# Kernel tuning notes

Measured on AMD Instinct MI355X. Metric: run time of the kernel, lower is better.

Reference implementation:

```python
import jax, jax.numpy as jnp
import numpy as np

NUM_HEADS = 8
SCALE = 25.0
SIM_THRESH = 0.75


def setup_inputs() -> dict:
    key = jax.random.key(0)
    ks = jax.random.split(key, 6)
    B, N, C = 1, 2048, 1024
    x_cls = jax.random.normal(ks[0], (B, N, C), jnp.float32)
    x_reg = jax.random.normal(ks[1], (B, N, C), jnp.float32)
    cls_score = jax.random.uniform(ks[2], (N,), jnp.float32)
    fg_score = jax.random.uniform(ks[3], (N,), jnp.float32)
    W_qkv_cls = jax.random.normal(ks[4], (3 * C, C), jnp.float32) * 0.02
    W_qkv_reg = jax.random.normal(ks[5], (3 * C, C), jnp.float32) * 0.02
    return {"x_cls": x_cls, "x_reg": x_reg, "cls_score": cls_score,
            "fg_score": fg_score, "W_qkv_cls": W_qkv_cls, "W_qkv_reg": W_qkv_reg}


def _l2norm(t):
    return t / jnp.linalg.norm(t, axis=-1, keepdims=True)


def reference(x_cls, x_reg, cls_score, fg_score, W_qkv_cls, W_qkv_reg):
    B, N, C = x_cls.shape
    H = NUM_HEADS
    d = C // H

    def qkv(x, W):
        # (B,N,3C) -> (3,B,H,N,d)
        t = (x @ W.T).reshape(B, N, 3, H, d).transpose(2, 0, 3, 1, 4)
        return t[0], t[1], t[2]

    q_cls, k_cls, v_cls = qkv(x_cls, W_qkv_cls)
    q_reg, k_reg, _ = qkv(x_reg, W_qkv_reg)

    q_cls, k_cls = _l2norm(q_cls), _l2norm(k_cls)
    q_reg, k_reg = _l2norm(q_reg), _l2norm(k_reg)
    v_cls_normed = _l2norm(v_cls)

    # scores broadcast: s[..., i, j] = score[j]; transpose -> score[i]
    s_cls = cls_score.reshape(1, 1, 1, N)
    s_fg = fg_score.reshape(1, 1, 1, N)
    # use_mask=True branch
    m_cls = (s_cls > jnp.swapaxes(s_cls, -2, -1) - 0.1).astype(x_cls.dtype)
    m_fg = (s_fg > jnp.swapaxes(s_fg, -2, -1) - 0.1).astype(x_cls.dtype)

    attn_cls_raw = jnp.einsum('bhid,bhjd->bhij', v_cls_normed, v_cls_normed)

    attn_cls = jax.nn.softmax(
        jnp.einsum('bhid,bhjd->bhij', q_cls, k_cls) * SCALE * s_cls * m_cls, axis=-1)
    attn_reg = jax.nn.softmax(
        jnp.einsum('bhid,bhjd->bhij', q_reg, k_reg) * SCALE * s_fg * m_fg, axis=-1)
    attn = (attn_reg + attn_cls) * 0.5

    x = jnp.einsum('bhij,bhjd->bhid', attn, v_cls).transpose(0, 2, 1, 3).reshape(B, N, C)
    x_ori = v_cls.transpose(0, 2, 1, 3).reshape(B, N, C)
    x_out = jnp.concatenate([x, x_ori], axis=-1)  # (B, N, 2C)

    # ave=True branch (batch 0, head-mean)
    raw = attn_cls_raw.sum(axis=1)[0] / H  # (N, N)
    sim_mask = (raw > SIM_THRESH).astype(x_cls.dtype)
    sim_attn = attn.sum(axis=1)[0] / H
    sim_round2 = jax.nn.softmax(sim_attn, axis=-1)
    sim_round2 = sim_mask * sim_round2
    sim_round2 = sim_round2 / jnp.sum(sim_round2, axis=-1, keepdims=True)
    return x_out, sim_round2
```

## Files before the change

kernel.cpp:

```cpp
#include <hip/hip_runtime.h>


#define NTOK 2048
#define CDIM 1024

typedef __attribute__((ext_vector_type(8))) short bf16x8;
typedef __attribute__((ext_vector_type(4))) short s16x4;
typedef __attribute__((ext_vector_type(2))) short s16x2;
typedef __attribute__((ext_vector_type(4))) float f32x4;

#define MFMA16(a,b,c) __builtin_amdgcn_mfma_f32_16x16x32_bf16((a),(b),(c),0,0,0)

__device__ __forceinline__ short f2bf(float x){
  unsigned u = __float_as_uint(x);
  u += 0x7FFFu + ((u >> 16) & 1u);
  return (short)(u >> 16);
}

__device__ __forceinline__ float bf2f(short s){
  return __uint_as_float(((unsigned)(unsigned short)s) << 16);
}

__device__ __forceinline__ int cvtpk(float lo, float hi){
  int r;
  asm("v_cvt_pk_bf16_f32 %0, %1, %2" : "=v"(r) : "v"(lo), "v"(hi));
  return r;
}

__device__ __forceinline__ void atomAddF(float* p, float v){
  unsafeAtomicAdd(p, v);
}

__device__ __forceinline__ void gld16(const short* g, short* l){
  __builtin_amdgcn_global_load_lds(
      (const __attribute__((address_space(1))) unsigned int*)g,
      (__attribute__((address_space(3))) unsigned int*)l, 16, 0, 0);
}

__global__ __launch_bounds__(256,8) void k_cvt(
    const float* __restrict__ xc, const float* __restrict__ xr,
    const float* __restrict__ Wc, const float* __restrict__ Wr,
    short* __restrict__ xbc, short* __restrict__ xbr,
    short* __restrict__ wbc, short* __restrict__ wbr)
{
  int idx = blockIdx.x*256 + threadIdx.x;
  const float* src; short* dst; int off;
  if      (idx <  262144){ src = xc; dst = xbc; off = idx; }
  else if (idx <  524288){ src = xr; dst = xbr; off = idx - 262144; }
  else if (idx <  917504){ src = Wc; dst = wbc; off = idx - 524288; }
  else                   { src = Wr; dst = wbr; off = idx - 917504; }
  float4 a = *(const float4*)(src + (size_t)off*8);
  float4 b = *(const float4*)(src + (size_t)off*8 + 4);
  bf16x8 o = { f2bf(a.x), f2bf(a.y), f2bf(a.z), f2bf(a.w),
               f2bf(b.x), f2bf(b.y), f2bf(b.z), f2bf(b.w) };
  *(bf16x8*)(dst + (size_t)off*8) = o;
}

__global__ __launch_bounds__(256,3) void k_qkv(
    const short* __restrict__ xbc, const short* __restrict__ xbr,
    const short* __restrict__ wbc, const short* __restrict__ wbr,
    short* __restrict__ qc, short* __restrict__ kc,
    short* __restrict__ qr, short* __restrict__ kr,
    short* __restrict__ vn, short* __restrict__ vb,
    float* __restrict__ out)
{
  const int tid = threadIdx.x;
  const int l   = tid & 63;
  const int w   = tid >> 6;
  const int fr  = l & 15;
  const int g   = l >> 4;
  const int fk8 = g * 8;

  const int L     = blockIdx.x;
  const int xcd   = L & 7;
  const int slot  = L >> 3;
  const int panel = xcd*5 + (slot >> 4);
  const int mb    = slot & 15;
  const int m0    = mb * 128;
  const int o0    = panel * 128;

  const short* Xb; const short* Wb; int wrow;
  if (o0 < 3072){ Xb = xbc; Wb = wbc; wrow = o0; }
  else          { Xb = xbr; Wb = wbr; wrow = o0 - 3072; }

  __shared__ __align__(16) short Ab[2][8][64][8];
  __shared__ __align__(16) short Bb[2][8][64][8];
  __shared__ float nbuf[128][2];

  const int wr = w >> 1;
  const int wc = w & 1;

#define QSTAGE(DB, KN) do {                                                  \
    _Pragma("unroll")                                                        \
    for (int it=0; it<2; ++it){                                              \
      int f = it*4 + w;                                                      \
      gld16(Xb + (size_t)(m0  + f*16 + fr)*CDIM + (KN) + fk8,                \
            &Ab[DB][f][0][0]);                                               \
      gld16(Wb + (size_t)(wrow + f*16 + fr)*CDIM + (KN) + fk8,               \
            &Bb[DB][f][0][0]);                                               \
    }                                                                        \
  } while(0)

  f32x4 acc[4][4] = {};

  QSTAGE(0, 0);
  __syncthreads();

  for (int kt = 0; kt < 32; ++kt){
    const int db = kt & 1;
    if (kt < 31){ if (db) QSTAGE(0, (kt+1)*32); else QSTAGE(1, (kt+1)*32); }
    bf16x8 af[4], bfr[4];
    #pragma unroll
    for (int ai=0;ai<4;ai++) af[ai]  = *(const bf16x8*)&Ab[db][wr*4+ai][l][0];
    #pragma unroll
    for (int bj=0;bj<4;bj++) bfr[bj] = *(const bf16x8*)&Bb[db][wc*4+bj][l][0];
    #pragma unroll
    for (int ai=0;ai<4;ai++)
      #pragma unroll
      for (int bj=0;bj<4;bj++)
        acc[ai][bj] = MFMA16(af[ai], bfr[bj], acc[ai][bj]);
    __syncthreads();
  }
#undef QSTAGE

  const int chunk = o0 >> 10;
  const int hh    = (o0 >> 7) & 7;

  float rn[4][4];
  #pragma unroll
  for (int ai=0;ai<4;ai++)
    #pragma unroll
    for (int r=0;r<4;r++){
      float ss = 0.f;
      #pragma unroll
      for (int bj=0;bj<4;bj++) ss += acc[ai][bj][r]*acc[ai][bj][r];
      ss += __shfl_xor(ss, 1); ss += __shfl_xor(ss, 2);
      ss += __shfl_xor(ss, 4); ss += __shfl_xor(ss, 8);
      if (fr == 0) nbuf[wr*64 + ai*16 + g*4 + r][wc] = ss;
      rn[ai][r] = ss;
    }
  __syncthreads();
  #pragma unroll
  for (int ai=0;ai<4;ai++)
    #pragma unroll
    for (int r=0;r<4;r++){
      int row = wr*64 + ai*16 + g*4 + r;
      rn[ai][r] = rsqrtf(nbuf[row][0] + nbuf[row][1]);
    }

  #pragma unroll
  for (int ai=0;ai<4;ai++)
    #pragma unroll
    for (int r=0;r<4;r++){
      int n   = m0 + wr*64 + ai*16 + g*4 + r;
      size_t base = ((size_t)hh*NTOK + n)*128;
      #pragma unroll
      for (int bj=0;bj<4;bj++){
        int col = wc*64 + bj*16 + fr;
        float val = acc[ai][bj][r];
        short nv  = f2bf(val * rn[ai][r]);
        switch(chunk){
          case 0: qc[base+col] = nv; break;
          case 1: kc[base+col] = nv; break;
          case 3: qr[base+col] = nv; break;
          case 4: kr[base+col] = nv; break;
          default:
            vn[base+col] = nv;
            vb[base+col] = f2bf(val);
            out[(size_t)n*2048 + 1024 + hh*128 + col] = val;
            break;
        }
      }
    }
}

__global__ __launch_bounds__(256,4) void k_vT(
    const short* __restrict__ vb, short* __restrict__ vT)
{
  int b = blockIdx.x;
  int h  = b >> 6;
  int nt = (b >> 1) & 31;
  int dt = b & 1;
  __shared__ short t[64][72];
  int tid = threadIdx.x;
  int r  = tid >> 2;
  int c0 = (tid & 3) << 4;
  #pragma unroll
  for (int u=0;u<2;u++){
    bf16x8 val = *(const bf16x8*)&vb[((size_t)h*NTOK + nt*64 + r)*128 + dt*64 + c0 + u*8];
    #pragma unroll
    for (int e=0;e<8;e++) t[r][c0+u*8+e] = val[e];
  }
  __syncthreads();
  #pragma unroll
  for (int u=0;u<2;u++){
    bf16x8 o;
    #pragma unroll
    for (int e=0;e<8;e++) o[e] = t[c0+u*8+e][r];
    *(bf16x8*)&vT[((size_t)h*128 + dt*64 + r)*NTOK + nt*64 + c0 + u*8] = o;
  }
}

#define JLEN 1024

__global__ __launch_bounds__(256,2) void k_attn(
    const short* __restrict__ qc, const short* __restrict__ kc,
    const short* __restrict__ qr, const short* __restrict__ kr,
    const short* __restrict__ vT,
    const float* __restrict__ csc, const float* __restrict__ fsc,
    float* __restrict__ s_cls, float* __restrict__ s_reg,
    short* __restrict__ Up)
{
  const int tid = threadIdx.x;
  const int l   = tid & 63;
  const int w   = tid >> 6;
  const int L    = blockIdx.x;
  const int xcd  = L & 7;
  const int slot = L >> 3;
  const int hs   = ((slot >> 5) << 3) | xcd;
  const int h    = hs >> 1;
  const int s    = hs & 1;
  const int rem  = slot & 31;
  const int js   = rem >> 4;
  const int ib   = rem & 15;

  const int iw  = ib * 128 + w * 32;
  const int fr  = l & 15;
  const int g   = l >> 4;
  const int fk8 = g * 8;
  const size_t hN = (size_t)h * NTOK;
  const size_t hD = (size_t)h * 128;

  const short* Qp = s ? qr : qc;
  const short* Kp = s ? kr : kc;
  const float* sc = s ? fsc : csc;
  float* ssum     = s ? s_reg : s_cls;
  short* Ub       = Up + (size_t)(js*2 + s) * 2097152;

  __shared__ __align__(16) short Kbuf[2][4][4][64][8];
  __shared__ __align__(16) short Vbuf[2][8][2][64][8];

  const int t8 = w * 8;

#define STAGE(DB, JN) do {                                                   \
    _Pragma("unroll")                                                        \
    for (int q8=0; q8<8; ++q8){                                              \
      int t = t8 + q8;                                                       \
      if (t < 16){                                                           \
        int jf = t >> 2, kk = t & 3;                                         \
        gld16(Kp + (hN + (JN) + jf*16 + fr)*128 + kk*32 + fk8,               \
              &Kbuf[DB][jf][kk][0][0]);                                      \
      } else {                                                               \
        int u = t - 16, df = u >> 1, ks = u & 1;                             \
        gld16(vT + (hD + df*16 + fr)*2048 + (JN) + ks*32 + fk8,              \
              &Vbuf[DB][df][ks][0][0]);                                      \
      }                                                                      \
    }                                                                        \
  } while(0)

  bf16x8 bq[2][4];
  #pragma unroll
  for (int i2=0;i2<2;i2++)
    #pragma unroll
    for (int kk=0;kk<4;kk++)
      bq[i2][kk] = *(const bf16x8*)&Qp[(hN + iw + i2*16 + fr)*128 + kk*32 + fk8];

  float sci[2];
  sci[0] = sc[iw + fr] - 0.1f;
  sci[1] = sc[iw + 16 + fr] - 0.1f;

  f32x4 U[2][8] = {};
  float p[2] = {0.f, 0.f};

  const int srcA = ((((g<<1)    & 3) << 4) + fr) << 2;
  const int srcB = ((((g<<1 | 1)& 3) << 4) + fr) << 2;
  const bool ghi = g >= 2;
  const int jbase = js * JLEN;

  STAGE(0, jbase);
  __syncthreads();

  for (int jt = 0; jt < 16; ++jt){
    const int db = jt & 1;
    const int j0 = jbase + jt*64;
    if (jt < 15){ if (db) STAGE(0, j0 + 64); else STAGE(1, j0 + 64); }
    #pragma unroll
    for (int ks=0; ks<2; ++ks){
      int cpk[2][2][2];
      #pragma unroll
      for (int t=0; t<2; ++t){
        const int jf = ks*2 + t;
        f32x4 S0 = {}; f32x4 S1 = {};
        __builtin_amdgcn_s_setprio(1);
        #pragma unroll
        for (int kk=0; kk<4; ++kk){
          bf16x8 kb = *(const bf16x8*)&Kbuf[db][jf][kk][l][0];
          S0 = MFMA16(kb, bq[0][kk], S0);
          S1 = MFMA16(kb, bq[1][kk], S1);
        }
        __builtin_amdgcn_s_setprio(0);
        float4 sjv = *(const float4*)&sc[j0 + jf*16 + 4*g];
        float e0[4], e1[4];
        #pragma unroll
        for (int r=0;r<4;r++){
          float sj = (&sjv.x)[r];
          float sj25 = 25.0f * sj;
          e0[r] = (sj > sci[0]) ? __expf(S0[r]*sj25) : 1.0f;
          e1[r] = (sj > sci[1]) ? __expf(S1[r]*sj25) : 1.0f;
          p[0] += e0[r]; p[1] += e1[r];
        }
        cpk[0][t][0] = cvtpk(e0[0], e0[1]);
        cpk[0][t][1] = cvtpk(e0[2], e0[3]);
        cpk[1][t][0] = cvtpk(e1[0], e1[1]);
        cpk[1][t][1] = cvtpk(e1[2], e1[3]);
      }
      bf16x8 ea[2];
      #pragma unroll
      for (int i2=0;i2<2;i2++){
        int a0 = __builtin_amdgcn_ds_bpermute(srcA, cpk[i2][0][0]);
        int a1 = __builtin_amdgcn_ds_bpermute(srcA, cpk[i2][0][1]);
        int a2 = __builtin_amdgcn_ds_bpermute(srcA, cpk[i2][1][0]);
        int a3 = __builtin_amdgcn_ds_bpermute(srcA, cpk[i2][1][1]);
        int b0 = __builtin_amdgcn_ds_bpermute(srcB, cpk[i2][0][0]);
        int b1 = __builtin_amdgcn_ds_bpermute(srcB, cpk[i2][0][1]);
        int b2 = __builtin_amdgcn_ds_bpermute(srcB, cpk[i2][1][0]);
        int b3 = __builtin_amdgcn_ds_bpermute(srcB, cpk[i2][1][1]);
        int wd[4];
        wd[0] = ghi ? a2 : a0;  wd[1] = ghi ? a3 : a1;
        wd[2] = ghi ? b2 : b0;  wd[3] = ghi ? b3 : b1;
        ea[i2] = *(bf16x8*)wd;
      }
      __builtin_amdgcn_s_setprio(1);
      #pragma unroll
      for (int df=0; df<8; ++df){
        bf16x8 bv = *(const bf16x8*)&Vbuf[db][df][ks][l][0];
        U[0][df] = MFMA16(ea[0], bv, U[0][df]);
        U[1][df] = MFMA16(ea[1], bv, U[1][df]);
      }
      __builtin_amdgcn_s_setprio(0);
    }
    __syncthreads();
  }
#undef STAGE

  #pragma unroll
  for (int i2=0;i2<2;i2++){
    p[i2] += __shfl_xor(p[i2], 16);
    p[i2] += __shfl_xor(p[i2], 32);
  }
  if (l < 16){
    atomAddF(&ssum[hN + iw + l],      p[0]);
    atomAddF(&ssum[hN + iw + 16 + l], p[1]);
  }
  #pragma unroll
  for (int i2=0;i2<2;i2++)
    #pragma unroll
    for (int df=0;df<8;df++)
      #pragma unroll
      for (int r=0;r<4;r++)
        Ub[(hN + iw + i2*16 + g*4 + r)*128 + df*16 + fr] = f2bf(U[i2][df][r]);
}

__global__ __launch_bounds__(256,8) void k_attn_fin(
    const short* __restrict__ Up,
    const float* __restrict__ s_cls, const float* __restrict__ s_reg,
    float* __restrict__ out)
{
  int task = blockIdx.x*4 + (threadIdx.x>>6);
  int lane = threadIdx.x & 63;
  int h = task >> 11;
  int row = task & 2047;
  size_t b = (size_t)task*128 + lane*2;
  float cx=0.f, cy=0.f, rx=0.f, ry=0.f;
  #pragma unroll
  for (int js=0; js<2; ++js){
    s16x2 c = *(const s16x2*)(Up + (size_t)(js*2+0)*2097152 + b);
    s16x2 r = *(const s16x2*)(Up + (size_t)(js*2+1)*2097152 + b);
    cx += bf2f(c[0]); cy += bf2f(c[1]);
    rx += bf2f(r[0]); ry += bf2f(r[1]);
  }
  float isc = 0.5f/s_cls[task];
  float isr = 0.5f/s_reg[task];
  float2 o = { cx*isc + rx*isr, cy*isc + ry*isr };
  *(float2*)&out[(size_t)row*2048 + h*128 + lane*2] = o;
}

__global__ __launch_bounds__(256,2) void k_sim(
    const short* __restrict__ qc, const short* __restrict__ kc,
    const short* __restrict__ qr, const short* __restrict__ kr,
    const float* __restrict__ csc, const float* __restrict__ fsc,
    const float* __restrict__ s_cls, const float* __restrict__ s_reg,
    float* __restrict__ out)
{
  const int tid  = threadIdx.x;
  const int lane = tid & 63;
  const int w    = tid >> 6;
  const int i0w  = blockIdx.x * 128 + w * 32;
  const int j0   = blockIdx.y * 64;
  const int fr   = lane & 15;
  const int fk   = (lane >> 4) * 8;

  __shared__ __align__(16) short Bsh[2][16][64][8];

  float sjc[4], sjf[4];
  #pragma unroll
  for (int js=0;js<4;js++){ sjc[js]=csc[j0+js*16+fr]; sjf[js]=fsc[j0+js*16+fr]; }
  int rowb[2]; float sci[2][4], sfi[2][4];
  #pragma unroll
  for (int ri=0;ri<2;ri++){
    rowb[ri] = i0w + ri*16 + ((lane>>4)<<2);
    #pragma unroll
    for (int r=0;r<4;r++){ sci[ri][r]=csc[rowb[ri]+r]; sfi[ri][r]=fsc[rowb[ri]+r]; }
  }

  f32x4 sim[2][4] = {};

  for (int h=0; h<8; ++h){
    const size_t hb = (size_t)h * NTOK;
    bf16x8 aq[2][4], ar[2][4];
    #pragma unroll
    for (int ri=0;ri<2;ri++)
      #pragma unroll
      for (int kk=0;kk<4;kk++){
        aq[ri][kk] = *(const bf16x8*)&qc[(hb + i0w + ri*16 + fr)*128 + kk*32 + fk];
        ar[ri][kk] = *(const bf16x8*)&qr[(hb + i0w + ri*16 + fr)*128 + kk*32 + fk];
      }
    float iscl[2][4], isrl[2][4];
    #pragma unroll
    for (int ri=0;ri<2;ri++)
      #pragma unroll
      for (int r=0;r<4;r++){
        iscl[ri][r] = 1.0f/s_cls[hb + rowb[ri] + r];
        isrl[ri][r] = 1.0f/s_reg[hb + rowb[ri] + r];
      }
    __syncthreads();
    #pragma unroll
    for (int it=0; it<8; ++it){
      int slot = it*256 + tid;
      int str  = slot >> 10;
      int frag = (slot >> 6) & 15;
      int l    = slot & 63;
      int r    = (frag >> 2)*16 + (l & 15);
      int c    = (frag & 3)*32 + (l >> 4)*8;
      const short* gp = (str ? kr : kc) + (hb + j0 + r)*128 + c;
      *(bf16x8*)&Bsh[str][frag][l][0] = *(const bf16x8*)gp;
    }
    __syncthreads();
    #pragma unroll
    for (int js=0; js<4; ++js){
      bf16x8 bc[4], br[4];
      #pragma unroll
      for (int kk=0;kk<4;kk++){
        bc[kk] = *(const bf16x8*)&Bsh[0][js*4+kk][lane][0];
        br[kk] = *(const bf16x8*)&Bsh[1][js*4+kk][lane][0];
      }
      #pragma unroll
      for (int ri=0;ri<2;ri++){
        f32x4 Sc = {}; f32x4 Sr = {};
        #pragma unroll
        for (int kk=0;kk<4;kk++){
          Sc = MFMA16(aq[ri][kk], bc[kk], Sc);
          Sr = MFMA16(ar[ri][kk], br[kk], Sr);
        }
        #pragma unroll
        for (int r=0;r<4;r++){
          float ec = (sjc[js] > sci[ri][r]-0.1f) ? __expf(Sc[r]*(25.0f*sjc[js])) : 1.0f;
          float er = (sjf[js] > sfi[ri][r]-0.1f) ? __expf(Sr[r]*(25.0f*sjf[js])) : 1.0f;
          sim[ri][js][r] += ec*iscl[ri][r] + er*isrl[ri][r];
        }
      }
    }
  }
  #pragma unroll
  for (int ri=0;ri<2;ri++)
    #pragma unroll
    for (int js=0;js<4;js++)
      #pragma unroll
      for (int r=0;r<4;r++)
        out[4194304ull + (size_t)(rowb[ri]+r)*2048 + j0 + js*16 + fr]
            = sim[ri][js][r] * 0.0625f;
}

__global__ __launch_bounds__(256,4) void k_raw(
    const short* __restrict__ vn, unsigned char* __restrict__ mask)
{
  const int tid  = threadIdx.x;
  const int lane = tid & 63;
  const int w    = tid >> 6;
  const int i0w  = blockIdx.x * 128 + w * 32;
  const int j0   = blockIdx.y * 64;
  const int fr   = lane & 15;
  const int fk   = (lane >> 4) * 8;

  __shared__ __align__(16) short Bsh[16][64][8];

  f32x4 raw[2][4] = {};

  for (int cc=0; cc<8; ++cc){
    const size_t hb = (size_t)cc * NTOK;
    bf16x8 av[2][4];
    #pragma unroll
    for (int ri=0;ri<2;ri++)
      #pragma unroll
      for (int kk=0;kk<4;kk++)
        av[ri][kk] = *(const bf16x8*)&vn[(hb + i0w + ri*16 + fr)*128 + kk*32 + fk];
    __syncthreads();
    #pragma unroll
    for (int it=0; it<4; ++it){
      int slot = it*256 + tid;
      int frag = (slot >> 6) & 15;
      int l    = slot & 63;
      int r    = (frag >> 2)*16 + (l & 15);
      int c    = (frag & 3)*32 + (l >> 4)*8;
      *(bf16x8*)&Bsh[frag][l][0] = *(const bf16x8*)&vn[(hb + j0 + r)*128 + c];
    }
    __syncthreads();
    #pragma unroll
    for (int js=0; js<4; ++js){
      bf16x8 bv[4];
      #pragma unroll
      for (int kk=0;kk<4;kk++) bv[kk] = *(const bf16x8*)&Bsh[js*4+kk][lane][0];
      #pragma unroll
      for (int ri=0;ri<2;ri++)
        #pragma unroll
        for (int kk=0;kk<4;kk++)
          raw[ri][js] = MFMA16(av[ri][kk], bv[kk], raw[ri][js]);
    }
  }
  const int rb0 = i0w + ((lane>>4)<<2);
  #pragma unroll
  for (int ri=0;ri<2;ri++)
    #pragma unroll
    for (int js=0;js<4;js++)
      #pragma unroll
      for (int r=0;r<4;r++)
        mask[(size_t)(rb0 + ri*16 + r)*2048 + j0 + js*16 + fr]
            = raw[ri][js][r] > 6.0f ? 1 : 0;
}

__global__ __launch_bounds__(256,4) void k_final(
    float* __restrict__ out, const unsigned char* __restrict__ mask)
{
  int row  = blockIdx.x*4 + (threadIdx.x>>6);
  int lane = threadIdx.x & 63;
  float* sr = out + 4194304ull + (size_t)row*2048;
  const unsigned char* mr = mask + (size_t)row*2048;
  float v[32];
  float sum2 = 0.0f;
  #pragma unroll
  for (int c=0;c<32;c++){
    float e = __expf(sr[c*64 + lane]);
    v[c] = (mr[c*64 + lane] != 0) ? e : 0.0f;
    sum2 += v[c];
  }
  #pragma unroll
  for (int m=1;m<64;m<<=1) sum2 += __shfl_xor(sum2, m);
  float inv = 1.0f / sum2;
  #pragma unroll
  for (int c=0;c<32;c++) sr[c*64 + lane] = v[c]*inv;
}

extern "C" void kernel_launch(void* const* d_in, const int* in_sizes, int n_in,
                              void* d_out, int out_size, void* d_ws, size_t ws_size,
                              hipStream_t stream)
{
  const float* xcls = (const float*)d_in[0];
  const float* xreg = (const float*)d_in[1];
  const float* csc  = (const float*)d_in[2];
  const float* fsc  = (const float*)d_in[3];
  const float* Wc   = (const float*)d_in[4];
  const float* Wr   = (const float*)d_in[5];
  float* out = (float*)d_out;

  char* ws = (char*)d_ws;
  short* xbc = (short*)ws;
  short* xbr = xbc + 2097152;
  short* wbc = xbr + 2097152;
  short* wbr = wbc + 3145728;
  unsigned char* mask = (unsigned char*)ws;
  char* accbase       = ws + 4u*1024*1024;
  float* s_cls        = (float*)(accbase);
  float* s_reg        = (float*)(accbase + 65536);
  short* Up           = (short*)(accbase + 131072);
  short* qc = (short*)(ws + 41943040ull);
  short* kc = qc + 2097152;
  short* qr = kc + 2097152;
  short* kr = qr + 2097152;
  short* vn = kr + 2097152;
  short* vb = vn + 2097152;
  short* vT = vb + 2097152;

  k_cvt  <<<4608,        256, 0, stream>>>(xcls, xreg, Wc, Wr, xbc, xbr, wbc, wbr);
  k_qkv  <<<640,         256, 0, stream>>>(xbc, xbr, wbc, wbr,
                                           qc, kc, qr, kr, vn, vb, out);
  k_vT   <<<512,         256, 0, stream>>>(vb, vT);
  hipMemsetAsync(accbase, 0, 131072, stream);
  k_attn <<<512,         256, 0, stream>>>(qc, kc, qr, kr, vT, csc, fsc,
                                           s_cls, s_reg, Up);
  k_attn_fin <<<4096,    256, 0, stream>>>(Up, s_cls, s_reg, out);
  k_raw  <<<dim3(16,32), 256, 0, stream>>>(vn, mask);
  k_sim  <<<dim3(16,32), 256, 0, stream>>>(qc, kc, qr, kr, csc, fsc, s_cls, s_reg, out);
  k_final<<<512,         256, 0, stream>>>(out, mask);
}
```

Measured before the change: 250.0 us.

## Fuse raw similarity mask into k_sim and widen k_attn to 8 waves

Removes the separate k_raw kernel by computing the V·V raw-similarity MFMAs inside k_sim, which now stages a third B tile (vn) in shared memory and writes the mask alongside the sim output. This drops a launch and reuses the existing tile loop and A-fragment loads. k_attn goes from 256 to 512 threads, each wave now owning 16 query rows instead of 32, with staging split over 8 waves. That should raise occupancy, but each K/V tile now feeds only one MFMA row block per load, and k_sim uses more registers and shared memory.

```diff
diff --git a/kernel.cpp b/kernel.cpp
--- a/kernel.cpp
+++ b/kernel.cpp
@@ -203,7 +203,7 @@
 
 #define JLEN 1024
 
-__global__ __launch_bounds__(256,2) void k_attn(
+__global__ __launch_bounds__(512,4) void k_attn(
     const short* __restrict__ qc, const short* __restrict__ kc,
     const short* __restrict__ qr, const short* __restrict__ kr,
     const short* __restrict__ vT,
@@ -224,7 +224,7 @@
   const int js   = rem >> 4;
   const int ib   = rem & 15;
 
-  const int iw  = ib * 128 + w * 32;
+  const int iw  = ib * 128 + w * 16;
   const int fr  = l & 15;
   const int g   = l >> 4;
   const int fk8 = g * 8;
@@ -240,12 +240,12 @@
   __shared__ __align__(16) short Kbuf[2][4][4][64][8];
   __shared__ __align__(16) short Vbuf[2][8][2][64][8];
 
-  const int t8 = w * 8;
+  const int t4 = w * 4;
 
 #define STAGE(DB, JN) do {                                                   \
     _Pragma("unroll")                                                        \
-    for (int q8=0; q8<8; ++q8){                                              \
-      int t = t8 + q8;                                                       \
+    for (int q4=0; q4<4; ++q4){                                              \
+      int t = t4 + q4;                                                       \
       if (t < 16){                                                           \
         int jf = t >> 2, kk = t & 3;                                         \
         gld16(Kp + (hN + (JN) + jf*16 + fr)*128 + kk*32 + fk8,               \
@@ -258,19 +258,15 @@
     }                                                                        \
   } while(0)
 
-  bf16x8 bq[2][4];
-  #pragma unroll
-  for (int i2=0;i2<2;i2++)
-    #pragma unroll
-    for (int kk=0;kk<4;kk++)
-      bq[i2][kk] = *(const bf16x8*)&Qp[(hN + iw + i2*16 + fr)*128 + kk*32 + fk8];
-
-  float sci[2];
-  sci[0] = sc[iw + fr] - 0.1f;
-  sci[1] = sc[iw + 16 + fr] - 0.1f;
-
-  f32x4 U[2][8] = {};
-  float p[2] = {0.f, 0.f};
+  bf16x8 bq[4];
+  #pragma unroll
+  for (int kk=0;kk<4;kk++)
+    bq[kk] = *(const bf16x8*)&Qp[(hN + iw + fr)*128 + kk*32 + fk8];
+
+  const float sci = sc[iw + fr] - 0.1f;
+
+  f32x4 U[8] = {};
+  float p = 0.f;
 
   const int srcA = ((((g<<1)    & 3) << 4) + fr) << 2;
   const int srcB = ((((g<<1 | 1)& 3) << 4) + fr) << 2;
@@ -286,56 +282,47 @@
     if (jt < 15){ if (db) STAGE(0, j0 + 64); else STAGE(1, j0 + 64); }
     #pragma unroll
     for (int ks=0; ks<2; ++ks){
-      int cpk[2][2][2];
+      int cpk[2][2];
       #pragma unroll
       for (int t=0; t<2; ++t){
         const int jf = ks*2 + t;
-        f32x4 S0 = {}; f32x4 S1 = {};
+        f32x4 S0 = {};
         __builtin_amdgcn_s_setprio(1);
         #pragma unroll
         for (int kk=0; kk<4; ++kk){
           bf16x8 kb = *(const bf16x8*)&Kbuf[db][jf][kk][l][0];
-          S0 = MFMA16(kb, bq[0][kk], S0);
-          S1 = MFMA16(kb, bq[1][kk], S1);
+          S0 = MFMA16(kb, bq[kk], S0);
         }
         __builtin_amdgcn_s_setprio(0);
         float4 sjv = *(const float4*)&sc[j0 + jf*16 + 4*g];
-        float e0[4], e1[4];
+        float e0[4];
         #pragma unroll
         for (int r=0;r<4;r++){
           float sj = (&sjv.x)[r];
           float sj25 = 25.0f * sj;
-          e0[r] = (sj > sci[0]) ? __expf(S0[r]*sj25) : 1.0f;
-          e1[r] = (sj > sci[1]) ? __expf(S1[r]*sj25) : 1.0f;
-          p[0] += e0[r]; p[1] += e1[r];
+          e0[r] = (sj > sci) ? __expf(S0[r]*sj25) : 1.0f;
+          p += e0[r];
         }
-        cpk[0][t][0] = cvtpk(e0[0], e0[1]);
-        cpk[0][t][1] = cvtpk(e0[2], e0[3]);
-        cpk[1][t][0] = cvtpk(e1[0], e1[1]);
-        cpk[1][t][1] = cvtpk(e1[2], e1[3]);
-      }
-      bf16x8 ea[2];
-      #pragma unroll
-      for (int i2=0;i2<2;i2++){
-        int a0 = __builtin_amdgcn_ds_bpermute(srcA, cpk[i2][0][0]);
-        int a1 = __builtin_amdgcn_ds_bpermute(srcA, cpk[i2][0][1]);
-        int a2 = __builtin_amdgcn_ds_bpermute(srcA, cpk[i2][1][0]);
-        int a3 = __builtin_amdgcn_ds_bpermute(srcA, cpk[i2][1][1]);
-        int b0 = __builtin_amdgcn_ds_bpermute(srcB, cpk[i2][0][0]);
-        int b1 = __builtin_amdgcn_ds_bpermute(srcB, cpk[i2][0][1]);
-        int b2 = __builtin_amdgcn_ds_bpermute(srcB, cpk[i2][1][0]);
-        int b3 = __builtin_amdgcn_ds_bpermute(srcB, cpk[i2][1][1]);
-        int wd[4];
-        wd[0] = ghi ? a2 : a0;  wd[1] = ghi ? a3 : a1;
-        wd[2] = ghi ? b2 : b0;  wd[3] = ghi ? b3 : b1;
-        ea[i2] = *(bf16x8*)wd;
-      }
+        cpk[t][0] = cvtpk(e0[0], e0[1]);
+        cpk[t][1] = cvtpk(e0[2], e0[3]);
+      }
+      int a0 = __builtin_amdgcn_ds_bpermute(srcA, cpk[0][0]);
+      int a1 = __builtin_amdgcn_ds_bpermute(srcA, cpk[0][1]);
+      int a2 = __builtin_amdgcn_ds_bpermute(srcA, cpk[1][0]);
+      int a3 = __builtin_amdgcn_ds_bpermute(srcA, cpk[1][1]);
+      int b0 = __builtin_amdgcn_ds_bpermute(srcB, cpk[0][0]);
+      int b1 = __builtin_amdgcn_ds_bpermute(srcB, cpk[0][1]);
+      int b2 = __builtin_amdgcn_ds_bpermute(srcB, cpk[1][0]);
+      int b3 = __builtin_amdgcn_ds_bpermute(srcB, cpk[1][1]);
+      int wd[4];
+      wd[0] = ghi ? a2 : a0;  wd[1] = ghi ? a3 : a1;
+      wd[2] = ghi ? b2 : b0;  wd[3] = ghi ? b3 : b1;
+      bf16x8 ea = *(bf16x8*)wd;
       __builtin_amdgcn_s_setprio(1);
       #pragma unroll
       for (int df=0; df<8; ++df){
         bf16x8 bv = *(const bf16x8*)&Vbuf[db][df][ks][l][0];
-        U[0][df] = MFMA16(ea[0], bv, U[0][df]);
-        U[1][df] = MFMA16(ea[1], bv, U[1][df]);
+        U[df] = MFMA16(ea, bv, U[df]);
       }
       __builtin_amdgcn_s_setprio(0);
     }
@@ -343,22 +330,15 @@
   }
 #undef STAGE
 
-  #pragma unroll
-  for (int i2=0;i2<2;i2++){
-    p[i2] += __shfl_xor(p[i2], 16);
-    p[i2] += __shfl_xor(p[i2], 32);
-  }
-  if (l < 16){
-    atomAddF(&ssum[hN + iw + l],      p[0]);
-    atomAddF(&ssum[hN + iw + 16 + l], p[1]);
-  }
-  #pragma unroll
-  for (int i2=0;i2<2;i2++)
-    #pragma unroll
-    for (int df=0;df<8;df++)
-      #pragma unroll
-      for (int r=0;r<4;r++)
-        Ub[(hN + iw + i2*16 + g*4 + r)*128 + df*16 + fr] = f2bf(U[i2][df][r]);
+  p += __shfl_xor(p, 16);
+  p += __shfl_xor(p, 32);
+  if (l < 16)
+    atomAddF(&ssum[hN + iw + l], p);
+  #pragma unroll
+  for (int df=0;df<8;df++)
+    #pragma unroll
+    for (int r=0;r<4;r++)
+      Ub[(hN + iw + g*4 + r)*128 + df*16 + fr] = f2bf(U[df][r]);
 }
 
 __global__ __launch_bounds__(256,8) void k_attn_fin(
@@ -388,9 +368,10 @@
 __global__ __launch_bounds__(256,2) void k_sim(
     const short* __restrict__ qc, const short* __restrict__ kc,
     const short* __restrict__ qr, const short* __restrict__ kr,
+    const short* __restrict__ vn,
     const float* __restrict__ csc, const float* __restrict__ fsc,
     const float* __restrict__ s_cls, const float* __restrict__ s_reg,
-    float* __restrict__ out)
+    unsigned char* __restrict__ mask, float* __restrict__ out)
 {
   const int tid  = threadIdx.x;
   const int lane = tid & 63;
@@ -400,7 +381,7 @@
   const int fr   = lane & 15;
   const int fk   = (lane >> 4) * 8;
 
-  __shared__ __align__(16) short Bsh[2][16][64][8];
+  __shared__ __align__(16) short Bsh[3][16][64][8];
 
   float sjc[4], sjf[4];
   #pragma unroll
@@ -414,16 +395,18 @@
   }
 
   f32x4 sim[2][4] = {};
+  f32x4 raw[2][4] = {};
 
   for (int h=0; h<8; ++h){
     const size_t hb = (size_t)h * NTOK;
-    bf16x8 aq[2][4], ar[2][4];
+    bf16x8 aq[2][4], ar[2][4], av[2][4];
     #pragma unroll
     for (int ri=0;ri<2;ri++)
       #pragma unroll
       for (int kk=0;kk<4;kk++){
         aq[ri][kk] = *(const bf16x8*)&qc[(hb + i0w + ri*16 + fr)*128 + kk*32 + fk];
         ar[ri][kk] = *(const bf16x8*)&qr[(hb + i0w + ri*16 + fr)*128 + kk*32 + fk];
+        av[ri][kk] = *(const bf16x8*)&vn[(hb + i0w + ri*16 + fr)*128 + kk*32 + fk];
       }
     float iscl[2][4], isrl[2][4];
     #pragma unroll
@@ -435,24 +418,25 @@
       }
     __syncthreads();
     #pragma unroll
-    for (int it=0; it<8; ++it){
+    for (int it=0; it<12; ++it){
       int slot = it*256 + tid;
       int str  = slot >> 10;
       int frag = (slot >> 6) & 15;
       int l    = slot & 63;
       int r    = (frag >> 2)*16 + (l & 15);
       int c    = (frag & 3)*32 + (l >> 4)*8;
-      const short* gp = (str ? kr : kc) + (hb + j0 + r)*128 + c;
+      const short* gp = (str==0 ? kc : (str==1 ? kr : vn)) + (hb + j0 + r)*128 + c;
       *(bf16x8*)&Bsh[str][frag][l][0] = *(const bf16x8*)gp;
     }
     __syncthreads();
     #pragma unroll
     for (int js=0; js<4; ++js){
-      bf16x8 bc[4], br[4];
+      bf16x8 bc[4], br[4], bv[4];
       #pragma unroll
       for (int kk=0;kk<4;kk++){
         bc[kk] = *(const bf16x8*)&Bsh[0][js*4+kk][lane][0];
         br[kk] = *(const bf16x8*)&Bsh[1][js*4+kk][lane][0];
+        bv[kk] = *(const bf16x8*)&Bsh[2][js*4+kk][lane][0];
       }
       #pragma unroll
       for (int ri=0;ri<2;ri++){
@@ -461,6 +445,7 @@
         for (int kk=0;kk<4;kk++){
           Sc = MFMA16(aq[ri][kk], bc[kk], Sc);
           Sr = MFMA16(ar[ri][kk], br[kk], Sr);
+          raw[ri][js] = MFMA16(av[ri][kk], bv[kk], raw[ri][js]);
         }
         #pragma unroll
         for (int r=0;r<4;r++){
@@ -476,66 +461,12 @@
     #pragma unroll
     for (int js=0;js<4;js++)
       #pragma unroll
-      for (int r=0;r<4;r++)
-        out[4194304ull + (size_t)(rowb[ri]+r)*2048 + j0 + js*16 + fr]
-            = sim[ri][js][r] * 0.0625f;
-}
-
-__global__ __launch_bounds__(256,4) void k_raw(
-    const short* __restrict__ vn, unsigned char* __restrict__ mask)
-{
-  const int tid  = threadIdx.x;
-  const int lane = tid & 63;
-  const int w    = tid >> 6;
-  const int i0w  = blockIdx.x * 128 + w * 32;
-  const int j0   = blockIdx.y * 64;
-  const int fr   = lane & 15;
-  const int fk   = (lane >> 4) * 8;
-
-  __shared__ __align__(16) short Bsh[16][64][8];
-
-  f32x4 raw[2][4] = {};
-
-  for (int cc=0; cc<8; ++cc){
-    const size_t hb = (size_t)cc * NTOK;
-    bf16x8 av[2][4];
-    #pragma unroll
-    for (int ri=0;ri<2;ri++)
-      #pragma unroll
-      for (int kk=0;kk<4;kk++)
-        av[ri][kk] = *(const bf16x8*)&vn[(hb + i0w + ri*16 + fr)*128 + kk*32 + fk];
-    __syncthreads();
-    #pragma unroll
-    for (int it=0; it<4; ++it){
-      int slot = it*256 + tid;
-      int frag = (slot >> 6) & 15;
-      int l    = slot & 63;
-      int r    = (frag >> 2)*16 + (l & 15);
-      int c    = (frag & 3)*32 + (l >> 4)*8;
-      *(bf16x8*)&Bsh[frag][l][0] = *(const bf16x8*)&vn[(hb + j0 + r)*128 + c];
-    }
-    __syncthreads();
-    #pragma unroll
-    for (int js=0; js<4; ++js){
-      bf16x8 bv[4];
-      #pragma unroll
-      for (int kk=0;kk<4;kk++) bv[kk] = *(const bf16x8*)&Bsh[js*4+kk][lane][0];
-      #pragma unroll
-      for (int ri=0;ri<2;ri++)
-        #pragma unroll
-        for (int kk=0;kk<4;kk++)
-          raw[ri][js] = MFMA16(av[ri][kk], bv[kk], raw[ri][js]);
-    }
-  }
-  const int rb0 = i0w + ((lane>>4)<<2);
-  #pragma unroll
-  for (int ri=0;ri<2;ri++)
-    #pragma unroll
-    for (int js=0;js<4;js++)
-      #pragma unroll
-      for (int r=0;r<4;r++)
-        mask[(size_t)(rb0 + ri*16 + r)*2048 + j0 + js*16 + fr]
-            = raw[ri][js][r] > 6.0f ? 1 : 0;
+      for (int r=0;r<4;r++){
+        int orow = rowb[ri] + r;
+        int ocol = j0 + js*16 + fr;
+        out[4194304ull + (size_t)orow*2048 + ocol] = sim[ri][js][r] * 0.0625f;
+        mask[(size_t)orow*2048 + ocol] = raw[ri][js][r] > 6.0f ? 1 : 0;
+      }
 }
 
 __global__ __launch_bounds__(256,4) void k_final(
@@ -595,10 +526,10 @@
                                            qc, kc, qr, kr, vn, vb, out);
   k_vT   <<<512,         256, 0, stream>>>(vb, vT);
   hipMemsetAsync(accbase, 0, 131072, stream);
-  k_attn <<<512,         256, 0, stream>>>(qc, kc, qr, kr, vT, csc, fsc,
+  k_attn <<<512,         512, 0, stream>>>(qc, kc, qr, kr, vT, csc, fsc,
                                            s_cls, s_reg, Up);
   k_attn_fin <<<4096,    256, 0, stream>>>(Up, s_cls, s_reg, out);
-  k_raw  <<<dim3(16,32), 256, 0, stream>>>(vn, mask);
-  k_sim  <<<dim3(16,32), 256, 0, stream>>>(qc, kc, qr, kr, csc, fsc, s_cls, s_reg, out);
+  k_sim  <<<dim3(16,32), 256, 0, stream>>>(qc, kc, qr, kr, vn, csc, fsc,
+                                           s_cls, s_reg, mask, out);
   k_final<<<512,         256, 0, stream>>>(out, mask);
 }
```

Result: slower. 255.1 us (+2.0%).
